# Performance work log

Measured on AMD Instinct MI355X. Metric: run time of the kernel, lower is better.

## Reference

```python
import jax, jax.numpy as jnp
import numpy as np

N = 50000   # nodes (= batch_size = num_e)
D = 256     # d_dim = n_hidden
E = 320000  # edges (first half 'in' direction, second half 'out'/inverse)
R = 400     # relation types (incl. inverses)


def setup_inputs() -> dict:
    key = jax.random.key(0)
    ks = jax.random.split(key, 12)
    s = 0.05  # weight scale so tanh stays in linear-ish range
    w = lambda k, shp: jax.random.normal(k, shp, jnp.float32) * s
    return {
        "emb": jax.random.normal(ks[0], (N, D), jnp.float32),
        "edge_index": jax.random.randint(ks[1], (2, E), 0, N),
        "edge_type": jax.random.randint(ks[2], (E,), 0, R),
        "rel1": w(ks[3], (R, D)),
        "W_in1": w(ks[4], (D, D)),
        "W_out1": w(ks[5], (D, D)),
        "W_loop1": w(ks[6], (D, D)),
        "b1": jnp.zeros((D,), jnp.float32),
        "rel2": w(ks[7], (R, D)),
        "W_in2": w(ks[8], (D, D)),
        "W_out2": w(ks[9], (D, D)),
        "W_loop2": w(ks[10], (D, D)),
        "b2": jnp.zeros((D,), jnp.float32),
        "res": jnp.array([0.1], jnp.float32),
        "mu_w": w(ks[11], (D, D)),
        "mu_b": jnp.zeros((D,), jnp.float32),
        "num_nodes": N,
    }


def _mgcn_conv(x, edge_index, edge_type, rel, W_in, W_out, W_loop, b, n):
    """Relational conv: gather -> compose with relation emb -> direction-split
    linear transform -> degree-normalized scatter-add -> self-loop -> tanh."""
    src, dst = edge_index[0], edge_index[1]
    e = edge_index.shape[1]
    half = e // 2
    m = x[src] * rel[edge_type]                                   # [E, D] compose ('mult')
    m = jnp.concatenate([m[:half] @ W_in, m[half:] @ W_out], 0)    # direction-specific transform
    deg = jax.ops.segment_sum(jnp.ones((e,), x.dtype), dst, num_segments=n)
    norm = 1.0 / jnp.maximum(deg, 1.0)                             # 1/in-degree
    agg = jax.ops.segment_sum(m * norm[dst][:, None], dst, num_segments=n)
    return jnp.tanh(agg + x @ W_loop + b)


def reference(emb, edge_index, edge_type,
              rel1, W_in1, W_out1, W_loop1, b1,
              rel2, W_in2, W_out2, W_loop2, b2,
              res, mu_w, mu_b, num_nodes):
    # forward_base with p.res=True, core_layer=2, dropout in eval mode (identity)
    h = emb + res * _mgcn_conv(emb, edge_index, edge_type, rel1, W_in1, W_out1, W_loop1, b1, num_nodes)
    h = h + res * _mgcn_conv(h, edge_index, edge_type, rel2, W_in2, W_out2, W_loop2, b2, num_nodes)
    # drift head f(t, y) = mu(forward_base(y))
    return h @ mu_w + mu_b
```

## Files before the change

kernel.cpp:

```cpp
#include <hip/hip_runtime.h>
#include <hip/hip_bf16.h>
#include <cstdint>
#include <cstddef>


typedef short bf16x8 __attribute__((ext_vector_type(8)));
typedef float f32x4  __attribute__((ext_vector_type(4)));

__device__ __forceinline__ float b2f(unsigned short u) {
    union { unsigned u32; float f; } c; c.u32 = ((unsigned)u) << 16; return c.f;
}
__device__ __forceinline__ unsigned short f2b(float f) {
    union { float f; unsigned u; } c; c.f = f;
    unsigned r = c.u + 0x7FFFu + ((c.u >> 16) & 1u);
    return (unsigned short)(r >> 16);
}
__device__ __forceinline__ float ftanh(float x) {
    float e = __expf(2.0f * x);
    return 1.0f - __fdividef(2.0f, e + 1.0f);
}


__global__ void k_hist(const int* __restrict__ dst, int* __restrict__ cnt, int E) {
    int i = blockIdx.x * blockDim.x + threadIdx.x;
    if (i < E) atomicAdd(&cnt[dst[i]], 1);
}

__global__ void k_norm(const int* __restrict__ cnt, float* __restrict__ norm, int N) {
    int i = blockIdx.x * blockDim.x + threadIdx.x;
    if (i < N) norm[i] = 1.0f / fmaxf((float)cnt[i], 1.0f);
}

__global__ void k_scan1(const int* __restrict__ cnt, int* __restrict__ part,
                        int* __restrict__ bsum, int N) {
    __shared__ int s[256];
    int i = blockIdx.x * 256 + threadIdx.x;
    int v = (i < N) ? cnt[i] : 0;
    s[threadIdx.x] = v; __syncthreads();
    #pragma unroll
    for (int o = 1; o < 256; o <<= 1) {
        int t = (threadIdx.x >= o) ? s[threadIdx.x - o] : 0;
        __syncthreads();
        s[threadIdx.x] += t;
        __syncthreads();
    }
    if (i < N) part[i] = s[threadIdx.x] - v;
    if (threadIdx.x == 255) bsum[blockIdx.x] = s[255];
}

__global__ void k_scan2(int* __restrict__ bsum, int nb) {
    __shared__ int s[256];
    int v = (threadIdx.x < nb) ? bsum[threadIdx.x] : 0;
    s[threadIdx.x] = v; __syncthreads();
    #pragma unroll
    for (int o = 1; o < 256; o <<= 1) {
        int t = (threadIdx.x >= o) ? s[threadIdx.x - o] : 0;
        __syncthreads();
        s[threadIdx.x] += t;
        __syncthreads();
    }
    if (threadIdx.x < nb) bsum[threadIdx.x] = s[threadIdx.x] - v;
}

__global__ void k_scan3(const int* __restrict__ part, const int* __restrict__ bsum,
                        int* __restrict__ rowptr, int* __restrict__ cursor, int N, int E) {
    int i = blockIdx.x * 256 + threadIdx.x;
    if (i < N) {
        int r = part[i] + bsum[blockIdx.x];
        rowptr[i] = r; cursor[i] = r;
    }
    if (i == 0) rowptr[N] = E;
}

__global__ void k_scatter(const int* __restrict__ src, const int* __restrict__ dst,
                          const int* __restrict__ et, int* __restrict__ cursor,
                          unsigned* __restrict__ erec, int E, int halfE) {
    int e = blockIdx.x * blockDim.x + threadIdx.x;
    if (e < E) {
        int d = dst[e];
        int pos = atomicAdd(&cursor[d], 1);
        unsigned rec = (unsigned)src[e] | ((unsigned)et[e] << 16)
                     | ((e >= halfE) ? 0x80000000u : 0u);
        erec[pos] = rec;
    }
}


__global__ void k_cvt3(const float* __restrict__ s0, unsigned short* __restrict__ d0, long n0,
                       const float* __restrict__ s1, unsigned short* __restrict__ d1, long n1,
                       const float* __restrict__ s2, unsigned short* __restrict__ d2, long n2) {
    long i = (long)blockIdx.x * blockDim.x + threadIdx.x;
    const float* s; unsigned short* d; long j = i;
    if (j < n0) { s = s0; d = d0; }
    else {
        j -= n0;
        if (j < n1) { s = s1; d = d1; }
        else { j -= n1; if (j >= n2) return; s = s2; d = d2; }
    }
    float4 v = ((const float4*)s)[j];
    ushort4 o;
    o.x = f2b(v.x); o.y = f2b(v.y); o.z = f2b(v.z); o.w = f2b(v.w);
    ((ushort4*)d)[j] = o;
}

__global__ void k_wfrag7(const float* __restrict__ w0, const float* __restrict__ w1,
                         const float* __restrict__ w2, const float* __restrict__ w3,
                         const float* __restrict__ w4, const float* __restrict__ w5,
                         const float* __restrict__ w6, unsigned short* __restrict__ out) {
    int o = blockIdx.x * 256 + threadIdx.x;
    int mi = o >> 16;
    int r  = o & 65535;
    const float* W = (mi == 0) ? w0 : (mi == 1) ? w1 : (mi == 2) ? w2 :
                     (mi == 3) ? w3 : (mi == 4) ? w4 : (mi == 5) ? w5 : w6;
    int j  = r & 7;
    int l  = (r >> 3) & 63;
    int nn = (r >> 9) & 15;
    int kg = r >> 13;
    int k = kg * 32 + (l >> 4) * 8 + j;
    int n = nn * 16 + (l & 15);
    out[o] = f2b(W[k * 256 + n]);
}


__global__ __launch_bounds__(256)
void k_agg(const unsigned short* __restrict__ xb, const unsigned short* __restrict__ relb,
           const int* __restrict__ rowptr, const unsigned* __restrict__ erec,
           const float* __restrict__ norm,
           unsigned short* __restrict__ sIn, unsigned short* __restrict__ sOut,
           int N, int D)
{
    const int w = threadIdx.x >> 6, l = threadIdx.x & 63;
    const int v = blockIdx.x * 4 + w;
    if (v >= N) return;
    const int rs = rowptr[v], re = rowptr[v + 1];
    const float nm = norm[v];

    float ai0 = 0, ai1 = 0, ai2 = 0, ai3 = 0;
    float ao0 = 0, ao1 = 0, ao2 = 0, ao3 = 0;

    unsigned c0 = (rs     < re) ? erec[rs]     : 0u;
    unsigned c1 = (rs + 1 < re) ? erec[rs + 1] : 0u;
    int i = rs;
    while (i + 2 <= re) {
        unsigned n0 = (i + 2 < re) ? erec[i + 2] : 0u;
        unsigned n1 = (i + 3 < re) ? erec[i + 3] : 0u;
        ushort4 x0 = *(const ushort4*)(xb   + (size_t)(c0 & 0xffff) * D + l * 4);
        ushort4 r0 = *(const ushort4*)(relb + (size_t)((c0 >> 16) & 0x7fff) * D + l * 4);
        ushort4 x1 = *(const ushort4*)(xb   + (size_t)(c1 & 0xffff) * D + l * 4);
        ushort4 r1 = *(const ushort4*)(relb + (size_t)((c1 >> 16) & 0x7fff) * D + l * 4);
        float p0 = b2f(x0.x) * b2f(r0.x), p1 = b2f(x0.y) * b2f(r0.y);
        float p2 = b2f(x0.z) * b2f(r0.z), p3 = b2f(x0.w) * b2f(r0.w);
        if (c0 >> 31) { ao0 += p0; ao1 += p1; ao2 += p2; ao3 += p3; }
        else          { ai0 += p0; ai1 += p1; ai2 += p2; ai3 += p3; }
        p0 = b2f(x1.x) * b2f(r1.x); p1 = b2f(x1.y) * b2f(r1.y);
        p2 = b2f(x1.z) * b2f(r1.z); p3 = b2f(x1.w) * b2f(r1.w);
        if (c1 >> 31) { ao0 += p0; ao1 += p1; ao2 += p2; ao3 += p3; }
        else          { ai0 += p0; ai1 += p1; ai2 += p2; ai3 += p3; }
        c0 = n0; c1 = n1; i += 2;
    }
    if (i < re) {
        ushort4 x0 = *(const ushort4*)(xb   + (size_t)(c0 & 0xffff) * D + l * 4);
        ushort4 r0 = *(const ushort4*)(relb + (size_t)((c0 >> 16) & 0x7fff) * D + l * 4);
        float p0 = b2f(x0.x) * b2f(r0.x), p1 = b2f(x0.y) * b2f(r0.y);
        float p2 = b2f(x0.z) * b2f(r0.z), p3 = b2f(x0.w) * b2f(r0.w);
        if (c0 >> 31) { ao0 += p0; ao1 += p1; ao2 += p2; ao3 += p3; }
        else          { ai0 += p0; ai1 += p1; ai2 += p2; ai3 += p3; }
    }

    ushort4 oi, oo;
    oi.x = f2b(ai0 * nm); oi.y = f2b(ai1 * nm); oi.z = f2b(ai2 * nm); oi.w = f2b(ai3 * nm);
    oo.x = f2b(ao0 * nm); oo.y = f2b(ao1 * nm); oo.z = f2b(ao2 * nm); oo.w = f2b(ao3 * nm);
    *(ushort4*)(sIn  + (size_t)v * D + l * 4) = oi;
    *(ushort4*)(sOut + (size_t)v * D + l * 4) = oo;
}


#define GITER(S, AtC, AtN, Rc0, Rc1, Rn0, Rn1)                                   \
  {                                                                              \
    const int p_ = (S) >> 2, cb_ = (S) & 3;                                      \
    const unsigned short* __restrict__ Wp_ = Wf + (size_t)p_ * 65536;            \
    _Pragma("unroll")                                                            \
    for (int kk = 0; kk < 2; ++kk) {                                             \
      const int kg_ = cb_ * 2 + kk;                                              \
      bf16x8 a_[4], b_[4];                                                       \
      _Pragma("unroll")                                                          \
      for (int m = 0; m < 4; ++m) {                                              \
        int rm = 16 * m + lr;                                                    \
        int ch = (kk * 4 + lq) ^ (rm & 7);                                       \
        a_[m] = *(const bf16x8*)(&AtC[rm * 64 + ch * 8]);                        \
      }                                                                          \
      _Pragma("unroll")                                                          \
      for (int n = 0; n < 4; ++n)                                                \
        b_[n] = *(const bf16x8*)(Wp_ + (((kg_ * 16 + (w * 4 + n)) * 64 + l) * 8));\
      _Pragma("unroll")                                                          \
      for (int m = 0; m < 4; ++m)                                                \
        _Pragma("unroll")                                                        \
        for (int n = 0; n < 4; ++n)                                              \
          acc[m][n] = __builtin_amdgcn_mfma_f32_16x16x32_bf16(a_[m], b_[n], acc[m][n], 0, 0, 0); \
    }                                                                            \
    if ((S) + 2 < NT) {                                                          \
      int p2_ = ((S) + 2) >> 2, cb2_ = ((S) + 2) & 3;                            \
      const unsigned short* ap_ = (p2_ == 0) ? a0 : ((p2_ == 1) ? a1 : a2);      \
      Rn0 = *(const uint4*)(ap_ + g0 + cb2_ * 64);                               \
      Rn1 = *(const uint4*)(ap_ + g1 + cb2_ * 64);                               \
    }                                                                            \
    if ((S) + 1 < NT) {                                                          \
      *(uint4*)(&AtN[wo0]) = Rc0;                                                \
      *(uint4*)(&AtN[wo1]) = Rc1;                                                \
    }                                                                            \
    asm volatile("s_waitcnt lgkmcnt(0)" ::: "memory");                           \
    __builtin_amdgcn_sched_barrier(0);                                           \
    __builtin_amdgcn_s_barrier();                                                \
    __builtin_amdgcn_sched_barrier(0);                                           \
  }

template <bool HEAD>
__global__ __launch_bounds__(256, 3)
void k_gemm(const unsigned short* __restrict__ a0,
            const unsigned short* __restrict__ a1,
            const unsigned short* __restrict__ a2,
            const unsigned short* __restrict__ Wf,
            const float* __restrict__ bias,
            const float* __restrict__ resPtr,
            const unsigned short* __restrict__ WfMu,
            const float* __restrict__ mub,
            float* __restrict__ outF,
            unsigned short* __restrict__ outB,
            int N, int D)
{
    __shared__ unsigned short lds[HEAD ? 16384 : 8192];
    unsigned short* At0 = lds;
    unsigned short* At1 = lds + 4096;

    const int t = threadIdx.x;
    const int rBase = blockIdx.x * 64;
    const int NT = 12;

    const int w  = t >> 6;
    const int l  = t & 63;
    const int lr = l & 15;
    const int lq = l >> 4;

    const int rS0 = t >> 3;
    const int rS1 = rS0 + 32;
    const int cS  = t & 7;
    const int wo0 = rS0 * 64 + ((cS ^ (rS0 & 7)) * 8);
    const int wo1 = rS1 * 64 + ((cS ^ (rS1 & 7)) * 8);
    const size_t g0 = (size_t)min(rBase + rS0, N - 1) * D + cS * 8;
    const size_t g1 = (size_t)min(rBase + rS1, N - 1) * D + cS * 8;

    f32x4 acc[4][4] = {};
    uint4 Ra0, Ra1, Rb0, Rb1;

    Ra0 = *(const uint4*)(a0 + g0);
    Ra1 = *(const uint4*)(a0 + g1);
    Rb0 = *(const uint4*)(a0 + g0 + 64);
    Rb1 = *(const uint4*)(a0 + g1 + 64);
    *(uint4*)(&At0[wo0]) = Ra0;
    *(uint4*)(&At0[wo1]) = Ra1;
    asm volatile("s_waitcnt lgkmcnt(0)" ::: "memory");
    __builtin_amdgcn_sched_barrier(0);
    __builtin_amdgcn_s_barrier();
    __builtin_amdgcn_sched_barrier(0);

    for (int s = 0; s < NT; s += 2) {
        GITER(s,     At0, At1, Rb0, Rb1, Ra0, Ra1);
        GITER(s + 1, At1, At0, Ra0, Ra1, Rb0, Rb1);
    }

    const int rb4 = lq * 4;
    const float resv = resPtr[0];
    #pragma unroll
    for (int m = 0; m < 4; ++m) {
        #pragma unroll
        for (int i = 0; i < 4; ++i) {
            int row = rBase + 16 * m + rb4 + i;
            if (row < N) {
                size_t base = (size_t)row * D + w * 64 + lr;
                int r6 = 16 * m + rb4 + i;
                #pragma unroll
                for (int n = 0; n < 4; ++n) {
                    int   c = w * 64 + lr + 16 * n;
                    float v = acc[m][n][i] + bias[c];
                    float h = b2f(a0[base + 16 * n]) + resv * ftanh(v);
                    if (HEAD) {
                        lds[r6 * 256 + (c ^ ((r6 & 7) << 3))] = f2b(h);
                    } else {
                        outB[base + 16 * n] = f2b(h);
                    }
                }
            }
        }
    }

    if (HEAD) {
        __syncthreads();
        #pragma unroll
        for (int m = 0; m < 4; ++m)
            #pragma unroll
            for (int n = 0; n < 4; ++n)
                acc[m][n] = (f32x4){0.f, 0.f, 0.f, 0.f};

        #pragma unroll
        for (int s2 = 0; s2 < 4; ++s2) {
            #pragma unroll
            for (int kk = 0; kk < 2; ++kk) {
                const int kg = s2 * 2 + kk;
                bf16x8 a_[4], b_[4];
                #pragma unroll
                for (int m = 0; m < 4; ++m) {
                    int rm = 16 * m + lr;
                    int ch = (s2 * 8 + kk * 4 + lq) ^ (rm & 7);
                    a_[m] = *(const bf16x8*)(&lds[rm * 256 + ch * 8]);
                }
                #pragma unroll
                for (int n = 0; n < 4; ++n)
                    b_[n] = *(const bf16x8*)(WfMu + (((kg * 16 + (w * 4 + n)) * 64 + l) * 8));
                #pragma unroll
                for (int m = 0; m < 4; ++m)
                    #pragma unroll
                    for (int n = 0; n < 4; ++n)
                        acc[m][n] = __builtin_amdgcn_mfma_f32_16x16x32_bf16(a_[m], b_[n], acc[m][n], 0, 0, 0);
            }
        }

        #pragma unroll
        for (int m = 0; m < 4; ++m) {
            #pragma unroll
            for (int i = 0; i < 4; ++i) {
                int row = rBase + 16 * m + rb4 + i;
                if (row < N) {
                    size_t base = (size_t)row * D + w * 64 + lr;
                    #pragma unroll
                    for (int n = 0; n < 4; ++n) {
                        int c = w * 64 + lr + 16 * n;
                        outF[base + 16 * n] = acc[m][n][i] + mub[c];
                    }
                }
            }
        }
    }
}


extern "C" void kernel_launch(void* const* d_in, const int* in_sizes, int n_in,
                              void* d_out, int out_size, void* d_ws, size_t ws_size,
                              hipStream_t stream)
{
    const float* emb  = (const float*)d_in[0];
    const int*   ei   = (const int*)  d_in[1];
    const int*   et   = (const int*)  d_in[2];
    const float* rel1 = (const float*)d_in[3];
    const float* Wi1  = (const float*)d_in[4];
    const float* Wo1  = (const float*)d_in[5];
    const float* Wl1  = (const float*)d_in[6];
    const float* b1   = (const float*)d_in[7];
    const float* rel2 = (const float*)d_in[8];
    const float* Wi2  = (const float*)d_in[9];
    const float* Wo2  = (const float*)d_in[10];
    const float* Wl2  = (const float*)d_in[11];
    const float* b2   = (const float*)d_in[12];
    const float* res  = (const float*)d_in[13];
    const float* muw  = (const float*)d_in[14];
    const float* mub  = (const float*)d_in[15];

    const int D = in_sizes[7];
    const int N = in_sizes[0] / D;
    const int E = in_sizes[2];
    const int R = in_sizes[3] / D;
    const int halfE = E / 2;
    const int* srcA = ei;
    const int* dstA = ei + E;
    const size_t DD = (size_t)D * D;

    char* ws = (char*)d_ws;
    size_t off = 0;
    auto alloc = [&](size_t bytes) -> char* {
        char* p = ws + off; off += (bytes + 255) & ~(size_t)255; return p;
    };
    const int nb1 = (N + 255) / 256;

    float*          norm   = (float*)          alloc((size_t)N * 4);
    int*            cnt    = (int*)            alloc((size_t)N * 4);
    int*            rowptr = (int*)            alloc((size_t)(N + 1) * 4);
    int*            cursor = (int*)            alloc((size_t)N * 4);
    int*            part   = (int*)            alloc((size_t)N * 4);
    int*            bsum   = (int*)            alloc(1024);
    unsigned*       erec   = (unsigned*)       alloc((size_t)E * 4);
    unsigned short* xb     = (unsigned short*) alloc((size_t)N * D * 2);
    unsigned short* h1b    = (unsigned short*) alloc((size_t)N * D * 2);
    unsigned short* sIn    = (unsigned short*) alloc((size_t)N * D * 2);
    unsigned short* sOut   = (unsigned short*) alloc((size_t)N * D * 2);
    unsigned short* r1b    = (unsigned short*) alloc((size_t)R * D * 2);
    unsigned short* r2b    = (unsigned short*) alloc((size_t)R * D * 2);
    unsigned short* fAll   = (unsigned short*) alloc(7 * DD * 2);
    if (off > ws_size) return;

    unsigned short* fW1 = fAll;
    unsigned short* fW2 = fAll + 3 * DD;
    unsigned short* fMu = fAll + 6 * DD;

    hipMemsetAsync(cnt, 0, (size_t)N * 4, stream);
    k_hist   <<<(E + 255) / 256, 256, 0, stream>>>(dstA, cnt, E);
    k_norm   <<<nb1, 256, 0, stream>>>(cnt, norm, N);
    k_scan1  <<<nb1, 256, 0, stream>>>(cnt, part, bsum, N);
    k_scan2  <<<1,   256, 0, stream>>>(bsum, nb1);
    k_scan3  <<<nb1, 256, 0, stream>>>(part, bsum, rowptr, cursor, N, E);
    k_scatter<<<(E + 255) / 256, 256, 0, stream>>>(srcA, dstA, et, cursor, erec, E, halfE);

    long nd4 = (long)N * D / 4, rd4 = (long)R * D / 4;
    long tot4 = nd4 + 2 * rd4;
    k_cvt3<<<(int)((tot4 + 255) / 256), 256, 0, stream>>>(
        emb, xb, nd4, rel1, r1b, rd4, rel2, r2b, rd4);
    k_wfrag7<<<(int)(7 * DD / 256), 256, 0, stream>>>(
        Wl1, Wi1, Wo1, Wl2, Wi2, Wo2, muw, fAll);

    const int AB = (N + 3) / 4;
    const int NB = (N + 63) / 64;

    k_agg<<<AB, 256, 0, stream>>>(xb, r1b, rowptr, erec, norm, sIn, sOut, N, D);
    k_gemm<false><<<NB, 256, 0, stream>>>(xb, sIn, sOut, fW1, b1, res,
                                          nullptr, nullptr, nullptr, h1b, N, D);

    k_agg<<<AB, 256, 0, stream>>>(h1b, r2b, rowptr, erec, norm, sIn, sOut, N, D);
    k_gemm<true><<<NB, 256, 0, stream>>>(h1b, sIn, sOut, fW2, b2, res,
                                         fMu, mub, (float*)d_out, nullptr, N, D);
}
```

Measured before the change: 243.6 us.

## Unroll edge aggregation by four, deepen GEMM prefetch, and stage epilogue stores through LDS

The aggregation kernel now processes four edges per iteration with lookahead index loads, which puts more gathers in flight per wave. The GEMM main loop uses three register stages, so global loads run two steps ahead. It is fully unrolled and the occupancy hint is raised from 3 to 4 blocks. Both epilogues now stage results in LDS and write coalesced 16-byte rows instead of scattered 2-byte or 4-byte stores. This adds extra barriers, two passes over LDS, and more register pressure, which may conflict with the higher occupancy target.

```diff
diff --git a/kernel.cpp b/kernel.cpp
--- a/kernel.cpp
+++ b/kernel.cpp
@@ -140,31 +140,52 @@
 
     unsigned c0 = (rs     < re) ? erec[rs]     : 0u;
     unsigned c1 = (rs + 1 < re) ? erec[rs + 1] : 0u;
+    unsigned c2 = (rs + 2 < re) ? erec[rs + 2] : 0u;
+    unsigned c3 = (rs + 3 < re) ? erec[rs + 3] : 0u;
     int i = rs;
-    while (i + 2 <= re) {
-        unsigned n0 = (i + 2 < re) ? erec[i + 2] : 0u;
-        unsigned n1 = (i + 3 < re) ? erec[i + 3] : 0u;
+    while (i + 4 <= re) {
+        unsigned m0 = (i + 4 < re) ? erec[i + 4] : 0u;
+        unsigned m1 = (i + 5 < re) ? erec[i + 5] : 0u;
+        unsigned m2 = (i + 6 < re) ? erec[i + 6] : 0u;
+        unsigned m3 = (i + 7 < re) ? erec[i + 7] : 0u;
         ushort4 x0 = *(const ushort4*)(xb   + (size_t)(c0 & 0xffff) * D + l * 4);
         ushort4 r0 = *(const ushort4*)(relb + (size_t)((c0 >> 16) & 0x7fff) * D + l * 4);
         ushort4 x1 = *(const ushort4*)(xb   + (size_t)(c1 & 0xffff) * D + l * 4);
         ushort4 r1 = *(const ushort4*)(relb + (size_t)((c1 >> 16) & 0x7fff) * D + l * 4);
-        float p0 = b2f(x0.x) * b2f(r0.x), p1 = b2f(x0.y) * b2f(r0.y);
-        float p2 = b2f(x0.z) * b2f(r0.z), p3 = b2f(x0.w) * b2f(r0.w);
+        ushort4 x2 = *(const ushort4*)(xb   + (size_t)(c2 & 0xffff) * D + l * 4);
+        ushort4 r2 = *(const ushort4*)(relb + (size_t)((c2 >> 16) & 0x7fff) * D + l * 4);
+        ushort4 x3 = *(const ushort4*)(xb   + (size_t)(c3 & 0xffff) * D + l * 4);
+        ushort4 r3 = *(const ushort4*)(relb + (size_t)((c3 >> 16) & 0x7fff) * D + l * 4);
+        float p0, p1, p2, p3;
+        p0 = b2f(x0.x)*b2f(r0.x); p1 = b2f(x0.y)*b2f(r0.y);
+        p2 = b2f(x0.z)*b2f(r0.z); p3 = b2f(x0.w)*b2f(r0.w);
         if (c0 >> 31) { ao0 += p0; ao1 += p1; ao2 += p2; ao3 += p3; }
         else          { ai0 += p0; ai1 += p1; ai2 += p2; ai3 += p3; }
-        p0 = b2f(x1.x) * b2f(r1.x); p1 = b2f(x1.y) * b2f(r1.y);
-        p2 = b2f(x1.z) * b2f(r1.z); p3 = b2f(x1.w) * b2f(r1.w);
+        p0 = b2f(x1.x)*b2f(r1.x); p1 = b2f(x1.y)*b2f(r1.y);
+        p2 = b2f(x1.z)*b2f(r1.z); p3 = b2f(x1.w)*b2f(r1.w);
         if (c1 >> 31) { ao0 += p0; ao1 += p1; ao2 += p2; ao3 += p3; }
         else          { ai0 += p0; ai1 += p1; ai2 += p2; ai3 += p3; }
-        c0 = n0; c1 = n1; i += 2;
-    }
-    if (i < re) {
-        ushort4 x0 = *(const ushort4*)(xb   + (size_t)(c0 & 0xffff) * D + l * 4);
-        ushort4 r0 = *(const ushort4*)(relb + (size_t)((c0 >> 16) & 0x7fff) * D + l * 4);
-        float p0 = b2f(x0.x) * b2f(r0.x), p1 = b2f(x0.y) * b2f(r0.y);
-        float p2 = b2f(x0.z) * b2f(r0.z), p3 = b2f(x0.w) * b2f(r0.w);
-        if (c0 >> 31) { ao0 += p0; ao1 += p1; ao2 += p2; ao3 += p3; }
+        p0 = b2f(x2.x)*b2f(r2.x); p1 = b2f(x2.y)*b2f(r2.y);
+        p2 = b2f(x2.z)*b2f(r2.z); p3 = b2f(x2.w)*b2f(r2.w);
+        if (c2 >> 31) { ao0 += p0; ao1 += p1; ao2 += p2; ao3 += p3; }
         else          { ai0 += p0; ai1 += p1; ai2 += p2; ai3 += p3; }
+        p0 = b2f(x3.x)*b2f(r3.x); p1 = b2f(x3.y)*b2f(r3.y);
+        p2 = b2f(x3.z)*b2f(r3.z); p3 = b2f(x3.w)*b2f(r3.w);
+        if (c3 >> 31) { ao0 += p0; ao1 += p1; ao2 += p2; ao3 += p3; }
+        else          { ai0 += p0; ai1 += p1; ai2 += p2; ai3 += p3; }
+        c0 = m0; c1 = m1; c2 = m2; c3 = m3; i += 4;
+    }
+    #pragma unroll
+    for (int j = 0; j < 3; ++j) {
+        if (i + j < re) {
+            unsigned cur = (j == 0) ? c0 : (j == 1) ? c1 : c2;
+            ushort4 x0 = *(const ushort4*)(xb   + (size_t)(cur & 0xffff) * D + l * 4);
+            ushort4 r0 = *(const ushort4*)(relb + (size_t)((cur >> 16) & 0x7fff) * D + l * 4);
+            float p0 = b2f(x0.x)*b2f(r0.x), p1 = b2f(x0.y)*b2f(r0.y);
+            float p2 = b2f(x0.z)*b2f(r0.z), p3 = b2f(x0.w)*b2f(r0.w);
+            if (cur >> 31) { ao0 += p0; ao1 += p1; ao2 += p2; ao3 += p3; }
+            else           { ai0 += p0; ai1 += p1; ai2 += p2; ai3 += p3; }
+        }
     }
 
     ushort4 oi, oo;
@@ -175,47 +196,52 @@
 }
 
 
-#define GITER(S, AtC, AtN, Rc0, Rc1, Rn0, Rn1)                                   \
-  {                                                                              \
-    const int p_ = (S) >> 2, cb_ = (S) & 3;                                      \
-    const unsigned short* __restrict__ Wp_ = Wf + (size_t)p_ * 65536;            \
-    _Pragma("unroll")                                                            \
-    for (int kk = 0; kk < 2; ++kk) {                                             \
-      const int kg_ = cb_ * 2 + kk;                                              \
-      bf16x8 a_[4], b_[4];                                                       \
-      _Pragma("unroll")                                                          \
-      for (int m = 0; m < 4; ++m) {                                              \
-        int rm = 16 * m + lr;                                                    \
-        int ch = (kk * 4 + lq) ^ (rm & 7);                                       \
-        a_[m] = *(const bf16x8*)(&AtC[rm * 64 + ch * 8]);                        \
-      }                                                                          \
-      _Pragma("unroll")                                                          \
-      for (int n = 0; n < 4; ++n)                                                \
-        b_[n] = *(const bf16x8*)(Wp_ + (((kg_ * 16 + (w * 4 + n)) * 64 + l) * 8));\
-      _Pragma("unroll")                                                          \
-      for (int m = 0; m < 4; ++m)                                                \
-        _Pragma("unroll")                                                        \
-        for (int n = 0; n < 4; ++n)                                              \
-          acc[m][n] = __builtin_amdgcn_mfma_f32_16x16x32_bf16(a_[m], b_[n], acc[m][n], 0, 0, 0); \
-    }                                                                            \
-    if ((S) + 2 < NT) {                                                          \
-      int p2_ = ((S) + 2) >> 2, cb2_ = ((S) + 2) & 3;                            \
-      const unsigned short* ap_ = (p2_ == 0) ? a0 : ((p2_ == 1) ? a1 : a2);      \
-      Rn0 = *(const uint4*)(ap_ + g0 + cb2_ * 64);                               \
-      Rn1 = *(const uint4*)(ap_ + g1 + cb2_ * 64);                               \
-    }                                                                            \
-    if ((S) + 1 < NT) {                                                          \
-      *(uint4*)(&AtN[wo0]) = Rc0;                                                \
-      *(uint4*)(&AtN[wo1]) = Rc1;                                                \
-    }                                                                            \
-    asm volatile("s_waitcnt lgkmcnt(0)" ::: "memory");                           \
-    __builtin_amdgcn_sched_barrier(0);                                           \
-    __builtin_amdgcn_s_barrier();                                                \
-    __builtin_amdgcn_sched_barrier(0);                                           \
-  }
+#define GIT(S, AtC, AtN, Rw0, Rw1, Rl0, Rl1)                                    \
+  do {                                                                          \
+    if ((S) + 1 < 12) {                                                         \
+      *(uint4*)(&AtN[wo0]) = Rw0;                                               \
+      *(uint4*)(&AtN[wo1]) = Rw1;                                               \
+    }                                                                           \
+    {                                                                           \
+      const int p_ = (S) >> 2, cb_ = (S) & 3;                                   \
+      const unsigned short* __restrict__ Wp_ = Wf + (size_t)p_ * 65536;         \
+      _Pragma("unroll")                                                         \
+      for (int kk_ = 0; kk_ < 2; ++kk_) {                                       \
+        const int kg_ = cb_ * 2 + kk_;                                          \
+        bf16x8 a_[4], b_[4];                                                    \
+        _Pragma("unroll")                                                       \
+        for (int m_ = 0; m_ < 4; ++m_) {                                        \
+          int rm_ = 16 * m_ + lr;                                               \
+          int ch_ = (kk_ * 4 + lq) ^ (rm_ & 7);                                 \
+          a_[m_] = *(const bf16x8*)(&AtC[rm_ * 64 + ch_ * 8]);                  \
+        }                                                                       \
+        _Pragma("unroll")                                                       \
+        for (int n_ = 0; n_ < 4; ++n_) {                                        \
+          b_[n_] = *(const bf16x8*)(Wp_ + (((kg_ * 16 + (w * 4 + n_)) * 64 + l) * 8)); \
+        }                                                                       \
+        _Pragma("unroll")                                                       \
+        for (int m_ = 0; m_ < 4; ++m_) {                                        \
+          _Pragma("unroll")                                                     \
+          for (int n_ = 0; n_ < 4; ++n_) {                                      \
+            acc[m_][n_] = __builtin_amdgcn_mfma_f32_16x16x32_bf16(a_[m_], b_[n_], acc[m_][n_], 0, 0, 0); \
+          }                                                                     \
+        }                                                                       \
+      }                                                                         \
+    }                                                                           \
+    if ((S) + 3 < 12) {                                                         \
+      const int p3_ = ((S) + 3) >> 2, cb3_ = ((S) + 3) & 3;                     \
+      const unsigned short* ap_ = (p3_ == 0) ? a0 : ((p3_ == 1) ? a1 : a2);     \
+      Rl0 = *(const uint4*)(ap_ + g0 + cb3_ * 64);                              \
+      Rl1 = *(const uint4*)(ap_ + g1 + cb3_ * 64);                              \
+    }                                                                           \
+    asm volatile("s_waitcnt lgkmcnt(0)" ::: "memory");                          \
+    __builtin_amdgcn_sched_barrier(0);                                          \
+    __builtin_amdgcn_s_barrier();                                               \
+    __builtin_amdgcn_sched_barrier(0);                                          \
+  } while (0)
 
 template <bool HEAD>
-__global__ __launch_bounds__(256, 3)
+__global__ __launch_bounds__(256, 4)
 void k_gemm(const unsigned short* __restrict__ a0,
             const unsigned short* __restrict__ a1,
             const unsigned short* __restrict__ a2,
@@ -234,7 +260,6 @@
 
     const int t = threadIdx.x;
     const int rBase = blockIdx.x * 64;
-    const int NT = 12;
 
     const int w  = t >> 6;
     const int l  = t & 63;
@@ -250,12 +275,14 @@
     const size_t g1 = (size_t)min(rBase + rS1, N - 1) * D + cS * 8;
 
     f32x4 acc[4][4] = {};
-    uint4 Ra0, Ra1, Rb0, Rb1;
+    uint4 Ra0, Ra1, Rb0, Rb1, Rc0, Rc1;
 
     Ra0 = *(const uint4*)(a0 + g0);
     Ra1 = *(const uint4*)(a0 + g1);
     Rb0 = *(const uint4*)(a0 + g0 + 64);
     Rb1 = *(const uint4*)(a0 + g1 + 64);
+    Rc0 = *(const uint4*)(a0 + g0 + 128);
+    Rc1 = *(const uint4*)(a0 + g1 + 128);
     *(uint4*)(&At0[wo0]) = Ra0;
     *(uint4*)(&At0[wo1]) = Ra1;
     asm volatile("s_waitcnt lgkmcnt(0)" ::: "memory");
@@ -263,43 +290,92 @@
     __builtin_amdgcn_s_barrier();
     __builtin_amdgcn_sched_barrier(0);
 
-    for (int s = 0; s < NT; s += 2) {
-        GITER(s,     At0, At1, Rb0, Rb1, Ra0, Ra1);
-        GITER(s + 1, At1, At0, Ra0, Ra1, Rb0, Rb1);
-    }
+    GIT(0,  At0, At1, Rb0, Rb1, Ra0, Ra1);
+    GIT(1,  At1, At0, Rc0, Rc1, Rb0, Rb1);
+    GIT(2,  At0, At1, Ra0, Ra1, Rc0, Rc1);
+    GIT(3,  At1, At0, Rb0, Rb1, Ra0, Ra1);
+    GIT(4,  At0, At1, Rc0, Rc1, Rb0, Rb1);
+    GIT(5,  At1, At0, Ra0, Ra1, Rc0, Rc1);
+    GIT(6,  At0, At1, Rb0, Rb1, Ra0, Ra1);
+    GIT(7,  At1, At0, Rc0, Rc1, Rb0, Rb1);
+    GIT(8,  At0, At1, Ra0, Ra1, Rc0, Rc1);
+    GIT(9,  At1, At0, Rb0, Rb1, Ra0, Ra1);
+    GIT(10, At0, At1, Rc0, Rc1, Rb0, Rb1);
+    GIT(11, At1, At0, Ra0, Ra1, Rc0, Rc1);
 
     const int rb4 = lq * 4;
     const float resv = resPtr[0];
-    #pragma unroll
-    for (int m = 0; m < 4; ++m) {
+
+    if (!HEAD) {
+        unsigned short* C = lds;
         #pragma unroll
-        for (int i = 0; i < 4; ++i) {
-            int row = rBase + 16 * m + rb4 + i;
-            if (row < N) {
-                size_t base = (size_t)row * D + w * 64 + lr;
-                int r6 = 16 * m + rb4 + i;
+        for (int half = 0; half < 2; ++half) {
+            if ((w >> 1) == half) {
                 #pragma unroll
-                for (int n = 0; n < 4; ++n) {
-                    int   c = w * 64 + lr + 16 * n;
-                    float v = acc[m][n][i] + bias[c];
-                    float h = b2f(a0[base + 16 * n]) + resv * ftanh(v);
-                    if (HEAD) {
+                for (int m = 0; m < 4; ++m) {
+                    #pragma unroll
+                    for (int i = 0; i < 4; ++i) {
+                        int r6 = 16 * m + rb4 + i;
+                        #pragma unroll
+                        for (int n = 0; n < 4; ++n) {
+                            int cH = (w & 1) * 64 + lr + 16 * n;
+                            float v = acc[m][n][i] + bias[half * 128 + cH];
+                            C[r6 * 128 + cH] = f2b(resv * ftanh(v));
+                        }
+                    }
+                }
+            }
+            __syncthreads();
+            #pragma unroll
+            for (int ii = 0; ii < 4; ++ii) {
+                int g   = ii * 256 + t;
+                int r   = g >> 4;
+                int cc  = g & 15;
+                int row = rBase + r;
+                if (row < N) {
+                    bf16x8 sv = *(const bf16x8*)(&C[r * 128 + cc * 8]);
+                    const unsigned short* ar = a0 + (size_t)row * D + half * 128 + cc * 8;
+                    uint4 av = *(const uint4*)ar;
+                    unsigned aw[4] = { av.x, av.y, av.z, av.w };
+                    unsigned ow[4];
+                    #pragma unroll
+                    for (int p = 0; p < 4; ++p) {
+                        float h0 = b2f((unsigned short)(aw[p] & 0xffff)) + b2f((unsigned short)sv[2 * p]);
+                        float h1 = b2f((unsigned short)(aw[p] >> 16))    + b2f((unsigned short)sv[2 * p + 1]);
+                        ow[p] = (unsigned)f2b(h0) | ((unsigned)f2b(h1) << 16);
+                    }
+                    *(uint4*)(outB + (size_t)row * D + half * 128 + cc * 8) =
+                        make_uint4(ow[0], ow[1], ow[2], ow[3]);
+                }
+            }
+            __syncthreads();
+        }
+    } else {
+        #pragma unroll
+        for (int m = 0; m < 4; ++m) {
+            #pragma unroll
+            for (int i = 0; i < 4; ++i) {
+                int row = rBase + 16 * m + rb4 + i;
+                if (row < N) {
+                    size_t base = (size_t)row * D + w * 64 + lr;
+                    int r6 = 16 * m + rb4 + i;
+                    #pragma unroll
+                    for (int n = 0; n < 4; ++n) {
+                        int   c = w * 64 + lr + 16 * n;
+                        float v = acc[m][n][i] + bias[c];
+                        float h = b2f(a0[base + 16 * n]) + resv * ftanh(v);
                         lds[r6 * 256 + (c ^ ((r6 & 7) << 3))] = f2b(h);
-                    } else {
-                        outB[base + 16 * n] = f2b(h);
                     }
                 }
             }
         }
-    }
-
-    if (HEAD) {
         __syncthreads();
         #pragma unroll
-        for (int m = 0; m < 4; ++m)
+        for (int m = 0; m < 4; ++m) {
             #pragma unroll
             for (int n = 0; n < 4; ++n)
                 acc[m][n] = (f32x4){0.f, 0.f, 0.f, 0.f};
+        }
 
         #pragma unroll
         for (int s2 = 0; s2 < 4; ++s2) {
@@ -317,27 +393,45 @@
                 for (int n = 0; n < 4; ++n)
                     b_[n] = *(const bf16x8*)(WfMu + (((kg * 16 + (w * 4 + n)) * 64 + l) * 8));
                 #pragma unroll
-                for (int m = 0; m < 4; ++m)
+                for (int m = 0; m < 4; ++m) {
                     #pragma unroll
                     for (int n = 0; n < 4; ++n)
                         acc[m][n] = __builtin_amdgcn_mfma_f32_16x16x32_bf16(a_[m], b_[n], acc[m][n], 0, 0, 0);
+                }
             }
         }
 
+        __syncthreads();
+        float* Cf = (float*)lds;
         #pragma unroll
-        for (int m = 0; m < 4; ++m) {
+        for (int half = 0; half < 2; ++half) {
+            if ((w >> 1) == half) {
+                #pragma unroll
+                for (int m = 0; m < 4; ++m) {
+                    #pragma unroll
+                    for (int i = 0; i < 4; ++i) {
+                        int r6 = 16 * m + rb4 + i;
+                        #pragma unroll
+                        for (int n = 0; n < 4; ++n) {
+                            int cH = (w & 1) * 64 + lr + 16 * n;
+                            Cf[r6 * 128 + cH] = acc[m][n][i] + mub[half * 128 + cH];
+                        }
+                    }
+                }
+            }
+            __syncthreads();
             #pragma unroll
-            for (int i = 0; i < 4; ++i) {
-                int row = rBase + 16 * m + rb4 + i;
+            for (int ii = 0; ii < 8; ++ii) {
+                int g   = ii * 256 + t;
+                int r   = g >> 5;
+                int cc  = g & 31;
+                int row = rBase + r;
                 if (row < N) {
-                    size_t base = (size_t)row * D + w * 64 + lr;
-                    #pragma unroll
-                    for (int n = 0; n < 4; ++n) {
-                        int c = w * 64 + lr + 16 * n;
-                        outF[base + 16 * n] = acc[m][n][i] + mub[c];
-                    }
+                    *(float4*)(outF + (size_t)row * D + half * 128 + cc * 4) =
+                        *(const float4*)(&Cf[r * 128 + cc * 4]);
                 }
             }
+            __syncthreads();
         }
     }
 }
```

Result: no change. 240.7 us (-1.2%).
